# Performance work log

Hardware: AMD Instinct MI355X
Metric: run time of the kernel (lower is better)

The kernel has to match this reference:

```python
import jax, jax.numpy as jnp
import numpy as np

DIM = 2048
N_HEADS = 16
N_KV_HEADS = 4
HEAD_DIM = DIM // N_HEADS  # 128
N_REP = N_HEADS // N_KV_HEADS
MAX_SEQ_LEN = 4096
SEQLEN = 4096


def setup_inputs() -> dict:
    key = jax.random.key(0)
    ks = jax.random.split(key, 6)
    x = jax.random.normal(ks[0], (1, SEQLEN, DIM), dtype=jnp.float32)
    # rotary frequencies, llama-style theta=10000
    inv_freq = 1.0 / (10000.0 ** (np.arange(0, HEAD_DIM, 2, dtype=np.float32) / HEAD_DIM))
    t = np.arange(SEQLEN, dtype=np.float32)
    ang = np.outer(t, inv_freq)  # [S, head_dim/2]
    freqs_cos = jnp.asarray(np.cos(ang))
    freqs_sin = jnp.asarray(np.sin(ang))
    # additive causal mask [S, S]
    mask = jnp.where(jnp.tril(jnp.ones((SEQLEN, SEQLEN), dtype=bool)), 0.0, -1e9).astype(jnp.float32)
    sc = 0.02
    wq = jax.random.normal(ks[1], (DIM, N_HEADS * HEAD_DIM), dtype=jnp.float32) * sc
    wk = jax.random.normal(ks[2], (DIM, N_KV_HEADS * HEAD_DIM), dtype=jnp.float32) * sc
    wv = jax.random.normal(ks[3], (DIM, N_KV_HEADS * HEAD_DIM), dtype=jnp.float32) * sc
    wo = jax.random.normal(ks[4], (N_HEADS * HEAD_DIM, DIM), dtype=jnp.float32) * sc
    return {"x": x, "start_pos": 0, "freqs_cos": freqs_cos, "freqs_sin": freqs_sin,
            "mask": mask, "wq": wq, "wk": wk, "wv": wv, "wo": wo}


def _rope(x, cos, sin):
    # x: [b, s, h, d]; cos/sin: [s, d/2]; consecutive pairs form complex numbers
    b, s, h, d = x.shape
    xr = x.astype(jnp.float32).reshape(b, s, h, d // 2, 2)
    x1, x2 = xr[..., 0], xr[..., 1]
    c = cos[None, :, None, :]
    sn = sin[None, :, None, :]
    o1 = x1 * c - x2 * sn
    o2 = x1 * sn + x2 * c
    return jnp.stack([o1, o2], axis=-1).reshape(b, s, h, d).astype(x.dtype)


def reference(x, start_pos, freqs_cos, freqs_sin, mask, wq, wk, wv, wo):
    bsz, seqlen, _ = x.shape
    xq = (x @ wq).reshape(bsz, seqlen, N_HEADS, HEAD_DIM)
    xk = (x @ wk).reshape(bsz, seqlen, N_KV_HEADS, HEAD_DIM)
    xv = (x @ wv).reshape(bsz, seqlen, N_KV_HEADS, HEAD_DIM)
    xq = _rope(xq, freqs_cos, freqs_sin)
    xk = _rope(xk, freqs_cos, freqs_sin)
    # KV-cache append (cache is zeros before this call)
    cache_k = jnp.zeros((1, MAX_SEQ_LEN, N_KV_HEADS, HEAD_DIM), dtype=xk.dtype)
    cache_v = jnp.zeros((1, MAX_SEQ_LEN, N_KV_HEADS, HEAD_DIM), dtype=xv.dtype)
    cache_k = jax.lax.dynamic_update_slice(cache_k, xk, (0, start_pos, 0, 0))
    cache_v = jax.lax.dynamic_update_slice(cache_v, xv, (0, start_pos, 0, 0))
    keys = cache_k[:bsz, : start_pos + seqlen]    # [b, T, kvh, d]
    values = cache_v[:bsz, : start_pos + seqlen]
    # GQA repeat to full head count
    keys = jnp.repeat(keys, N_REP, axis=2)
    values = jnp.repeat(values, N_REP, axis=2)
    scale = 1.0 / jnp.sqrt(jnp.float32(HEAD_DIM))
    scores = jnp.einsum('bshd,bthd->bhst', xq, keys) * scale  # [b, h, s, T]
    scores = scores + mask[None, None, :, :]
    probs = jax.nn.softmax(scores.astype(jnp.float32), axis=-1).astype(xq.dtype)
    out = jnp.einsum('bhst,bthd->bshd', probs, values).reshape(bsz, seqlen, -1)
    return out @ wo
```

## Files before the change

### kernel.cpp

```cpp
#include <hip/hip_runtime.h>
#include <hip/hip_bf16.h>
#include <stdint.h>

#define SEQ 4096
#define DIM 2048
#define NH 16
#define NKV 4
#define HD 128
#define KVLD 1024


using frag8 = __attribute__((ext_vector_type(8))) short;
using f32x4 = __attribute__((ext_vector_type(4))) float;

union VecU { ushort u[8]; uint4 v; };

__device__ __forceinline__ float bf2f(ushort u) {
    union { uint32_t u; float f; } v; v.u = ((uint32_t)u) << 16; return v.f;
}
__device__ __forceinline__ ushort f2bf(float f) {
    union { float f; uint32_t u; } v; v.f = f;
    uint32_t r = v.u + 0x7fffu + ((v.u >> 16) & 1u);
    return (ushort)(r >> 16);
}

__device__ __forceinline__ void glds16(const void* g, void* l) {
    __builtin_amdgcn_global_load_lds(
        (const __attribute__((address_space(1))) void*)g,
        (__attribute__((address_space(3))) void*)l, 16, 0, 0);
}

__global__ __launch_bounds__(256) void cvt_kernel(
    const float* __restrict__ src, ushort* __restrict__ dst)
{
    size_t i = ((size_t)blockIdx.x * 256 + threadIdx.x) * 8;
    float4 f0 = *(const float4*)&src[i];
    float4 f1 = *(const float4*)&src[i + 4];
    VecU t;
    t.u[0] = f2bf(f0.x); t.u[1] = f2bf(f0.y); t.u[2] = f2bf(f0.z); t.u[3] = f2bf(f0.w);
    t.u[4] = f2bf(f1.x); t.u[5] = f2bf(f1.y); t.u[6] = f2bf(f1.z); t.u[7] = f2bf(f1.w);
    *(uint4*)&dst[i] = t.v;
}

__global__ __launch_bounds__(256) void convT_kernel(
    const float* __restrict__ src, ushort* __restrict__ dst, int K, int N)
{
    __shared__ ushort T[32][36];
    int r  = threadIdx.x >> 3;
    int c4 = (threadIdx.x & 7) * 4;
    int bk = blockIdx.y * 32, bn = blockIdx.x * 32;
    float4 v = *(const float4*)&src[(size_t)(bk + r) * N + bn + c4];
    T[r][c4]     = f2bf(v.x); T[r][c4 + 1] = f2bf(v.y);
    T[r][c4 + 2] = f2bf(v.z); T[r][c4 + 3] = f2bf(v.w);
    __syncthreads();
    ushort4 o;
    o.x = T[c4][r]; o.y = T[c4 + 1][r]; o.z = T[c4 + 2][r]; o.w = T[c4 + 3][r];
    *(ushort4*)&dst[(size_t)(bn + r) * K + bk + c4] = o;
}

__global__ __launch_bounds__(256) void vtrans_kernel(
    const ushort* __restrict__ src, ushort* __restrict__ dst)
{
    __shared__ ushort T[32][36];
    int r  = threadIdx.x >> 3;
    int c4 = (threadIdx.x & 7) * 4;
    int bt = blockIdx.y * 32, bd = blockIdx.x * 32;
    ushort4 v = *(const ushort4*)&src[(size_t)(bt + r) * KVLD + 512 + bd + c4];
    T[r][c4] = v.x; T[r][c4 + 1] = v.y; T[r][c4 + 2] = v.z; T[r][c4 + 3] = v.w;
    __syncthreads();
    ushort4 o;
    o.x = T[c4][r]; o.y = T[c4 + 1][r]; o.z = T[c4 + 2][r]; o.w = T[c4 + 3][r];
    *(ushort4*)&dst[(size_t)(bd + r) * SEQ + bt + c4] = o;
}

template <int CF>
__global__ __launch_bounds__(256) void gemm_tn(
    const ushort* __restrict__ A, const ushort* __restrict__ BT,
    void* __restrict__ C, int M, int N, int K)
{
    __shared__ ushort As[128 * 32];
    __shared__ ushort Bs[128 * 32];

    const int tid  = threadIdx.x;
    const int lane = tid & 63;
    const int wave = tid >> 6;
    const int bm   = blockIdx.y * 128;
    const int bn   = blockIdx.x * 128;
    const int wm   = (wave >> 1) * 64;
    const int wn   = (wave & 1) * 64;
    const int quad = lane >> 4;
    const int t16  = lane & 15;
    const int kg   = quad ^ ((t16 >> 1) & 3);

    f32x4 acc[4][4] = {};

    for (int k0 = 0; k0 < K; k0 += 32) {
        #pragma unroll
        for (int it = 0; it < 2; ++it) {
            int gid = it * 256 + tid;
            int r   = gid >> 2;
            int cs  = (gid & 3) ^ ((gid >> 3) & 3);
            glds16(&A[(size_t)(bm + r) * K + k0 + cs * 8],
                   &As[(it * 256 + wave * 64) * 8]);
            glds16(&BT[(size_t)(bn + r) * K + k0 + cs * 8],
                   &Bs[(it * 256 + wave * 64) * 8]);
        }
        __syncthreads();

        frag8 af[4], bf[4];
        #pragma unroll
        for (int i = 0; i < 4; ++i)
            af[i] = *(const frag8*)&As[(wm + i * 16 + t16) * 32 + kg * 8];
        #pragma unroll
        for (int j = 0; j < 4; ++j)
            bf[j] = *(const frag8*)&Bs[(wn + j * 16 + t16) * 32 + kg * 8];
        #pragma unroll
        for (int i = 0; i < 4; ++i)
            #pragma unroll
            for (int j = 0; j < 4; ++j)
                acc[i][j] = __builtin_amdgcn_mfma_f32_16x16x32_bf16(
                    af[i], bf[j], acc[i][j], 0, 0, 0);
        __syncthreads();
    }

    #pragma unroll
    for (int i = 0; i < 4; ++i)
        #pragma unroll
        for (int j = 0; j < 4; ++j)
            #pragma unroll
            for (int r = 0; r < 4; ++r) {
                int row = bm + wm + i * 16 + quad * 4 + r;
                int col = bn + wn + j * 16 + t16;
                if (CF) ((float*)C)[(size_t)row * N + col] = acc[i][j][r];
                else    ((ushort*)C)[(size_t)row * N + col] = f2bf(acc[i][j][r]);
            }
}

__global__ void rope_kernel(ushort* __restrict__ X, const float* __restrict__ Cos,
                            const float* __restrict__ Sin, int log2nh, int strideT,
                            float oscale)
{
    int idx = blockIdx.x * blockDim.x + threadIdx.x;
    int p = idx & 63;
    int h = (idx >> 6) & ((1 << log2nh) - 1);
    int t = idx >> (6 + log2nh);
    size_t base = (size_t)t * strideT + (size_t)h * 128 + 2 * p;
    ushort2 xv = *(ushort2*)&X[base];
    float x1 = bf2f(xv.x), x2 = bf2f(xv.y);
    float c = Cos[t * 64 + p], s = Sin[t * 64 + p];
    ushort2 ov;
    ov.x = f2bf((x1 * c - x2 * s) * oscale);
    ov.y = f2bf((x1 * s + x2 * c) * oscale);
    *(ushort2*)&X[base] = ov;
}

__global__ __launch_bounds__(256) void attn_kernel(
    const ushort* __restrict__ Q, const ushort* __restrict__ Kb,
    const ushort* __restrict__ VT, ushort* __restrict__ O)
{
    __shared__ ushort Ks[64][136];
    __shared__ ushort Vt[128][72];
    __shared__ ushort Sp[4][16][72];

    const int tid  = threadIdx.x;
    const int lane = tid & 63;
    const int wave = tid >> 6;
    const int quad = lane >> 4;
    const int t16  = lane & 15;
    const int h    = blockIdx.y;
    const int kvh  = h >> 2;

    frag8 vONE;
    #pragma unroll
    for (int i = 0; i < 8; ++i) vONE[i] = (short)0x3F80;

    #pragma unroll
    for (int qi = 0; qi < 2; ++qi) {
        const int qt = qi ? (63 - (int)blockIdx.x) : (int)blockIdx.x;
        const int q0 = qt * 64;
        const int qwave = q0 + wave * 16;
        const int qmaxw = qwave + 15;

        frag8 aQ[4];
        #pragma unroll
        for (int kk = 0; kk < 4; ++kk)
            aQ[kk] = *(const frag8*)&Q[(size_t)(qwave + t16) * DIM + h * HD + kk * 32 + quad * 8];

        f32x4 o[8] = {};
        f32x4 o9 = {0.f, 0.f, 0.f, 0.f};
        float mrow[4];
        #pragma unroll
        for (int r = 0; r < 4; ++r) mrow[r] = -30000.f;

        for (int t0 = 0; t0 <= q0 + 63; t0 += 64) {
            #pragma unroll
            for (int it = 0; it < 4; ++it) {
                int idx = tid + it * 256;
                int tt  = idx >> 4;
                int c   = (idx & 15) * 8;
                *(uint4*)&Ks[tt][c] =
                    *(const uint4*)&Kb[(size_t)(t0 + tt) * KVLD + kvh * HD + c];
            }
            #pragma unroll
            for (int it = 0; it < 4; ++it) {
                int idx = tid + it * 256;
                int d   = idx >> 3;
                int tq  = (idx & 7) * 8;
                *(uint4*)&Vt[d][tq] =
                    *(const uint4*)&VT[(size_t)(kvh * HD + d) * SEQ + t0 + tq];
            }
            __syncthreads();

            const bool hi = (t0 + 32 <= qmaxw);
            {
                f32x4 s0 = {0.f, 0.f, 0.f, 0.f};
                f32x4 s1 = {0.f, 0.f, 0.f, 0.f};
                f32x4 s2 = {0.f, 0.f, 0.f, 0.f};
                f32x4 s3 = {0.f, 0.f, 0.f, 0.f};
                #pragma unroll
                for (int kk = 0; kk < 4; ++kk) {
                    frag8 b0 = *(const frag8*)&Ks[2 * t16][kk * 32 + quad * 8];
                    frag8 b1 = *(const frag8*)&Ks[2 * t16 + 1][kk * 32 + quad * 8];
                    s0 = __builtin_amdgcn_mfma_f32_16x16x32_bf16(aQ[kk], b0, s0, 0, 0, 0);
                    s1 = __builtin_amdgcn_mfma_f32_16x16x32_bf16(aQ[kk], b1, s1, 0, 0, 0);
                }
                if (hi) {
                    #pragma unroll
                    for (int kk = 0; kk < 4; ++kk) {
                        frag8 b2 = *(const frag8*)&Ks[32 + 2 * t16][kk * 32 + quad * 8];
                        frag8 b3 = *(const frag8*)&Ks[33 + 2 * t16][kk * 32 + quad * 8];
                        s2 = __builtin_amdgcn_mfma_f32_16x16x32_bf16(aQ[kk], b2, s2, 0, 0, 0);
                        s3 = __builtin_amdgcn_mfma_f32_16x16x32_bf16(aQ[kk], b3, s3, 0, 0, 0);
                    }
                }

                const bool mLo = (t0 + 31 > qwave);
                const bool mHi = (t0 + 63 > qwave);
                float v[4][4];
                float mnew[4];
                bool trig = false;
                #pragma unroll
                for (int r = 0; r < 4; ++r) {
                    int q = qwave + quad * 4 + r;
                    float v0 = s0[r];
                    float v1 = s1[r];
                    float v2 = hi ? s2[r] : -30000.f;
                    float v3 = hi ? s3[r] : -30000.f;
                    if (mLo) {
                        if (t0 + 2 * t16 > q)      v0 = -30000.f;
                        if (t0 + 2 * t16 + 1 > q)  v1 = -30000.f;
                    }
                    if (hi && mHi) {
                        if (t0 + 32 + 2 * t16 > q) v2 = -30000.f;
                        if (t0 + 33 + 2 * t16 > q) v3 = -30000.f;
                    }
                    float rm = fmaxf(fmaxf(v0, v1), fmaxf(v2, v3));
                    rm = fmaxf(rm, __shfl_xor(rm, 1));
                    rm = fmaxf(rm, __shfl_xor(rm, 2));
                    rm = fmaxf(rm, __shfl_xor(rm, 4));
                    rm = fmaxf(rm, __shfl_xor(rm, 8));
                    mnew[r] = fmaxf(mrow[r], rm);
                    trig |= (rm > mrow[r] + 8.f);
                    v[r][0] = v0; v[r][1] = v1; v[r][2] = v2; v[r][3] = v3;
                }
                if (__any(trig)) {
                    #pragma unroll
                    for (int r = 0; r < 4; ++r) {
                        float alpha = __expf(mrow[r] - mnew[r]);
                        mrow[r] = mnew[r];
                        #pragma unroll
                        for (int j = 0; j < 8; ++j) o[j][r] *= alpha;
                        o9[r] *= alpha;
                    }
                }
                #pragma unroll
                for (int r = 0; r < 4; ++r) {
                    float e0 = __expf(v[r][0] - mrow[r]);
                    float e1 = __expf(v[r][1] - mrow[r]);
                    uint pv = (uint)f2bf(e0) | ((uint)f2bf(e1) << 16);
                    *(uint*)&Sp[wave][quad * 4 + r][2 * t16] = pv;
                    if (hi) {
                        float e2 = __expf(v[r][2] - mrow[r]);
                        float e3 = __expf(v[r][3] - mrow[r]);
                        uint ph = (uint)f2bf(e2) | ((uint)f2bf(e3) << 16);
                        *(uint*)&Sp[wave][quad * 4 + r][32 + 2 * t16] = ph;
                    }
                }

                frag8 aP0 = *(const frag8*)&Sp[wave][t16][quad * 8];
                #pragma unroll
                for (int j = 0; j < 8; ++j) {
                    frag8 bV = *(const frag8*)&Vt[j * 16 + t16][quad * 8];
                    o[j] = __builtin_amdgcn_mfma_f32_16x16x32_bf16(aP0, bV, o[j], 0, 0, 0);
                }
                o9 = __builtin_amdgcn_mfma_f32_16x16x32_bf16(aP0, vONE, o9, 0, 0, 0);
                if (hi) {
                    frag8 aP1 = *(const frag8*)&Sp[wave][t16][32 + quad * 8];
                    #pragma unroll
                    for (int j = 0; j < 8; ++j) {
                        frag8 bV = *(const frag8*)&Vt[j * 16 + t16][32 + quad * 8];
                        o[j] = __builtin_amdgcn_mfma_f32_16x16x32_bf16(aP1, bV, o[j], 0, 0, 0);
                    }
                    o9 = __builtin_amdgcn_mfma_f32_16x16x32_bf16(aP1, vONE, o9, 0, 0, 0);
                }
            }
            __syncthreads();
        }

        #pragma unroll
        for (int r = 0; r < 4; ++r) {
            float inv = 1.f / fmaxf(o9[r], 1e-20f);
            int row = qwave + quad * 4 + r;
            #pragma unroll
            for (int j = 0; j < 8; ++j)
                O[(size_t)row * DIM + h * HD + j * 16 + t16] = f2bf(o[j][r] * inv);
        }
    }
}

extern "C" void kernel_launch(void* const* d_in, const int* in_sizes, int n_in,
                              void* d_out, int out_size, void* d_ws, size_t ws_size,
                              hipStream_t stream)
{
    const float* x  = (const float*)d_in[0];
    const float* fc = (const float*)d_in[2];
    const float* fs = (const float*)d_in[3];
    const float* wq = (const float*)d_in[5];
    const float* wk = (const float*)d_in[6];
    const float* wv = (const float*)d_in[7];
    const float* wo = (const float*)d_in[8];

    ushort* Qb  = (ushort*)d_ws;
    ushort* KVb = Qb + (size_t)SEQ * DIM;
    ushort* Ab  = KVb + (size_t)SEQ * KVLD;
    ushort* WqT = Ab;
    ushort* KVT = Ab + (size_t)DIM * DIM;
    ushort* WoT = KVb;

    ushort* Xb = (ushort*)d_out;
    ushort* VT = Xb + (size_t)SEQ * DIM;

    dim3 blk(256);

    cvt_kernel<<<(SEQ * DIM) / 2048, blk, 0, stream>>>(x, Xb);
    convT_kernel<<<dim3(DIM / 32, DIM / 32), blk, 0, stream>>>(wq, WqT, DIM, DIM);
    convT_kernel<<<dim3(512 / 32, DIM / 32), blk, 0, stream>>>(wk, KVT, DIM, 512);
    convT_kernel<<<dim3(512 / 32, DIM / 32), blk, 0, stream>>>(
        wv, KVT + (size_t)512 * DIM, DIM, 512);

    gemm_tn<0><<<dim3(DIM / 128, SEQ / 128), blk, 0, stream>>>(Xb, WqT, Qb, SEQ, DIM, DIM);
    gemm_tn<0><<<dim3(KVLD / 128, SEQ / 128), blk, 0, stream>>>(Xb, KVT, KVb, SEQ, KVLD, DIM);

    rope_kernel<<<(SEQ * NH * 64) / 256, blk, 0, stream>>>(
        Qb, fc, fs, 4, DIM, 0.08838834764831845f);
    rope_kernel<<<(SEQ * NKV * 64) / 256, blk, 0, stream>>>(
        KVb, fc, fs, 2, KVLD, 1.0f);

    vtrans_kernel<<<dim3(512 / 32, SEQ / 32), blk, 0, stream>>>(KVb, VT);

    attn_kernel<<<dim3(32, NH), blk, 0, stream>>>(Qb, KVb, VT, Ab);

    convT_kernel<<<dim3(DIM / 32, DIM / 32), blk, 0, stream>>>(wo, WoT, DIM, DIM);
    gemm_tn<1><<<dim3(DIM / 128, SEQ / 128), blk, 0, stream>>>(Ab, WoT, d_out, SEQ, DIM, DIM);
}
```

Before: 502.9 us.

## Prefetch next K/V tile into registers and defer row-max reduction to rare rescale path

The attention loop now issues global loads for the next K and V tile into registers before computing the current tile, then writes them to shared memory after the current tile's MFMAs. This overlaps global memory latency with compute. The running max starts at zero and the cross-lane max reduction and rescale run only when some lane's local max exceeds the running max by a threshold, in which case exponentials are recomputed. This saves shuffles on the common path but costs extra registers and an additional barrier per tile.

```diff
diff --git a/kernel.cpp b/kernel.cpp
--- a/kernel.cpp
+++ b/kernel.cpp
@@ -174,12 +174,43 @@
     #pragma unroll
     for (int i = 0; i < 8; ++i) vONE[i] = (short)0x3F80;
 
+#define LOADREGS(T0)                                                          \
+    {                                                                         \
+        _Pragma("unroll")                                                     \
+        for (int it = 0; it < 4; ++it) {                                      \
+            int idx = tid + it * 256;                                         \
+            kreg[it] = *(const uint4*)&Kb[(size_t)((T0) + (idx >> 4)) * KVLD  \
+                                          + kvh * HD + (idx & 15) * 8];       \
+        }                                                                     \
+        _Pragma("unroll")                                                     \
+        for (int it = 0; it < 4; ++it) {                                      \
+            int idx = tid + it * 256;                                         \
+            vreg[it] = *(const uint4*)&VT[(size_t)(kvh * HD + (idx >> 3)) * SEQ \
+                                          + (T0) + (idx & 7) * 8];            \
+        }                                                                     \
+    }
+
+#define WRITELDS()                                                            \
+    {                                                                         \
+        _Pragma("unroll")                                                     \
+        for (int it = 0; it < 4; ++it) {                                      \
+            int idx = tid + it * 256;                                         \
+            *(uint4*)&Ks[idx >> 4][(idx & 15) * 8] = kreg[it];                \
+        }                                                                     \
+        _Pragma("unroll")                                                     \
+        for (int it = 0; it < 4; ++it) {                                      \
+            int idx = tid + it * 256;                                         \
+            *(uint4*)&Vt[idx >> 3][(idx & 7) * 8] = vreg[it];                 \
+        }                                                                     \
+    }
+
     #pragma unroll
     for (int qi = 0; qi < 2; ++qi) {
         const int qt = qi ? (63 - (int)blockIdx.x) : (int)blockIdx.x;
         const int q0 = qt * 64;
         const int qwave = q0 + wave * 16;
         const int qmaxw = qwave + 15;
+        const int ntiles = qt + 1;
 
         frag8 aQ[4];
         #pragma unroll
@@ -188,62 +219,80 @@
 
         f32x4 o[8] = {};
         f32x4 o9 = {0.f, 0.f, 0.f, 0.f};
-        float mrow[4];
-        #pragma unroll
-        for (int r = 0; r < 4; ++r) mrow[r] = -30000.f;
-
-        for (int t0 = 0; t0 <= q0 + 63; t0 += 64) {
-            #pragma unroll
-            for (int it = 0; it < 4; ++it) {
-                int idx = tid + it * 256;
-                int tt  = idx >> 4;
-                int c   = (idx & 15) * 8;
-                *(uint4*)&Ks[tt][c] =
-                    *(const uint4*)&Kb[(size_t)(t0 + tt) * KVLD + kvh * HD + c];
-            }
-            #pragma unroll
-            for (int it = 0; it < 4; ++it) {
-                int idx = tid + it * 256;
-                int d   = idx >> 3;
-                int tq  = (idx & 7) * 8;
-                *(uint4*)&Vt[d][tq] =
-                    *(const uint4*)&VT[(size_t)(kvh * HD + d) * SEQ + t0 + tq];
-            }
-            __syncthreads();
+        float mrow[4] = {0.f, 0.f, 0.f, 0.f};
+
+        uint4 kreg[4], vreg[4];
+
+        LOADREGS(0);
+        WRITELDS();
+        __syncthreads();
+
+        for (int ti = 0; ti < ntiles; ++ti) {
+            const int t0 = ti * 64;
+
+            if (ti + 1 < ntiles) LOADREGS((ti + 1) * 64);
 
             const bool hi = (t0 + 32 <= qmaxw);
-            {
-                f32x4 s0 = {0.f, 0.f, 0.f, 0.f};
-                f32x4 s1 = {0.f, 0.f, 0.f, 0.f};
-                f32x4 s2 = {0.f, 0.f, 0.f, 0.f};
-                f32x4 s3 = {0.f, 0.f, 0.f, 0.f};
+
+            f32x4 s0 = {0.f, 0.f, 0.f, 0.f};
+            f32x4 s1 = {0.f, 0.f, 0.f, 0.f};
+            f32x4 s2 = {0.f, 0.f, 0.f, 0.f};
+            f32x4 s3 = {0.f, 0.f, 0.f, 0.f};
+            #pragma unroll
+            for (int kk = 0; kk < 4; ++kk) {
+                frag8 b0 = *(const frag8*)&Ks[2 * t16][kk * 32 + quad * 8];
+                frag8 b1 = *(const frag8*)&Ks[2 * t16 + 1][kk * 32 + quad * 8];
+                s0 = __builtin_amdgcn_mfma_f32_16x16x32_bf16(aQ[kk], b0, s0, 0, 0, 0);
+                s1 = __builtin_amdgcn_mfma_f32_16x16x32_bf16(aQ[kk], b1, s1, 0, 0, 0);
+            }
+            if (hi) {
                 #pragma unroll
                 for (int kk = 0; kk < 4; ++kk) {
-                    frag8 b0 = *(const frag8*)&Ks[2 * t16][kk * 32 + quad * 8];
-                    frag8 b1 = *(const frag8*)&Ks[2 * t16 + 1][kk * 32 + quad * 8];
-                    s0 = __builtin_amdgcn_mfma_f32_16x16x32_bf16(aQ[kk], b0, s0, 0, 0, 0);
-                    s1 = __builtin_amdgcn_mfma_f32_16x16x32_bf16(aQ[kk], b1, s1, 0, 0, 0);
-                }
+                    frag8 b2 = *(const frag8*)&Ks[32 + 2 * t16][kk * 32 + quad * 8];
+                    frag8 b3 = *(const frag8*)&Ks[33 + 2 * t16][kk * 32 + quad * 8];
+                    s2 = __builtin_amdgcn_mfma_f32_16x16x32_bf16(aQ[kk], b2, s2, 0, 0, 0);
+                    s3 = __builtin_amdgcn_mfma_f32_16x16x32_bf16(aQ[kk], b3, s3, 0, 0, 0);
+                }
+            }
+
+            const bool mLo = (t0 + 31 > qwave);
+            const bool mHi = (t0 + 63 > qwave);
+
+            bool trig = false;
+            #pragma unroll
+            for (int r = 0; r < 4; ++r) {
+                int q = qwave + quad * 4 + r;
+                float v0 = s0[r];
+                float v1 = s1[r];
+                float v2 = hi ? s2[r] : -30000.f;
+                float v3 = hi ? s3[r] : -30000.f;
+                if (mLo) {
+                    if (t0 + 2 * t16 > q)      v0 = -30000.f;
+                    if (t0 + 2 * t16 + 1 > q)  v1 = -30000.f;
+                }
+                if (hi && mHi) {
+                    if (t0 + 32 + 2 * t16 > q) v2 = -30000.f;
+                    if (t0 + 33 + 2 * t16 > q) v3 = -30000.f;
+                }
+                float lm = fmaxf(fmaxf(v0, v1), fmaxf(v2, v3));
+                trig |= (lm > mrow[r] + 8.f);
+                float e0 = __expf(v0 - mrow[r]);
+                float e1 = __expf(v1 - mrow[r]);
+                *(uint*)&Sp[wave][quad * 4 + r][2 * t16] =
+                    (uint)f2bf(e0) | ((uint)f2bf(e1) << 16);
                 if (hi) {
-                    #pragma unroll
-                    for (int kk = 0; kk < 4; ++kk) {
-                        frag8 b2 = *(const frag8*)&Ks[32 + 2 * t16][kk * 32 + quad * 8];
-                        frag8 b3 = *(const frag8*)&Ks[33 + 2 * t16][kk * 32 + quad * 8];
-                        s2 = __builtin_amdgcn_mfma_f32_16x16x32_bf16(aQ[kk], b2, s2, 0, 0, 0);
-                        s3 = __builtin_amdgcn_mfma_f32_16x16x32_bf16(aQ[kk], b3, s3, 0, 0, 0);
-                    }
-                }
-
-                const bool mLo = (t0 + 31 > qwave);
-                const bool mHi = (t0 + 63 > qwave);
-                float v[4][4];
-                float mnew[4];
-                bool trig = false;
+                    float e2 = __expf(v2 - mrow[r]);
+                    float e3 = __expf(v3 - mrow[r]);
+                    *(uint*)&Sp[wave][quad * 4 + r][32 + 2 * t16] =
+                        (uint)f2bf(e2) | ((uint)f2bf(e3) << 16);
+                }
+            }
+
+            if (__any(trig)) {
                 #pragma unroll
                 for (int r = 0; r < 4; ++r) {
                     int q = qwave + quad * 4 + r;
-                    float v0 = s0[r];
-                    float v1 = s1[r];
+                    float v0 = s0[r], v1 = s1[r];
                     float v2 = hi ? s2[r] : -30000.f;
                     float v3 = hi ? s3[r] : -30000.f;
                     if (mLo) {
@@ -259,52 +308,47 @@
                     rm = fmaxf(rm, __shfl_xor(rm, 2));
                     rm = fmaxf(rm, __shfl_xor(rm, 4));
                     rm = fmaxf(rm, __shfl_xor(rm, 8));
-                    mnew[r] = fmaxf(mrow[r], rm);
-                    trig |= (rm > mrow[r] + 8.f);
-                    v[r][0] = v0; v[r][1] = v1; v[r][2] = v2; v[r][3] = v3;
-                }
-                if (__any(trig)) {
+                    float mnew  = fmaxf(mrow[r], rm);
+                    float alpha = __expf(mrow[r] - mnew);
                     #pragma unroll
-                    for (int r = 0; r < 4; ++r) {
-                        float alpha = __expf(mrow[r] - mnew[r]);
-                        mrow[r] = mnew[r];
-                        #pragma unroll
-                        for (int j = 0; j < 8; ++j) o[j][r] *= alpha;
-                        o9[r] *= alpha;
+                    for (int j = 0; j < 8; ++j) o[j][r] *= alpha;
+                    o9[r] *= alpha;
+                    mrow[r] = mnew;
+                    float e0 = __expf(v0 - mnew);
+                    float e1 = __expf(v1 - mnew);
+                    *(uint*)&Sp[wave][quad * 4 + r][2 * t16] =
+                        (uint)f2bf(e0) | ((uint)f2bf(e1) << 16);
+                    if (hi) {
+                        float e2 = __expf(v2 - mnew);
+                        float e3 = __expf(v3 - mnew);
+                        *(uint*)&Sp[wave][quad * 4 + r][32 + 2 * t16] =
+                            (uint)f2bf(e2) | ((uint)f2bf(e3) << 16);
                     }
                 }
-                #pragma unroll
-                for (int r = 0; r < 4; ++r) {
-                    float e0 = __expf(v[r][0] - mrow[r]);
-                    float e1 = __expf(v[r][1] - mrow[r]);
-                    uint pv = (uint)f2bf(e0) | ((uint)f2bf(e1) << 16);
-                    *(uint*)&Sp[wave][quad * 4 + r][2 * t16] = pv;
-                    if (hi) {
-                        float e2 = __expf(v[r][2] - mrow[r]);
-                        float e3 = __expf(v[r][3] - mrow[r]);
-                        uint ph = (uint)f2bf(e2) | ((uint)f2bf(e3) << 16);
-                        *(uint*)&Sp[wave][quad * 4 + r][32 + 2 * t16] = ph;
-                    }
-                }
-
-                frag8 aP0 = *(const frag8*)&Sp[wave][t16][quad * 8];
+            }
+
+            frag8 aP0 = *(const frag8*)&Sp[wave][t16][quad * 8];
+            #pragma unroll
+            for (int j = 0; j < 8; ++j) {
+                frag8 bV = *(const frag8*)&Vt[j * 16 + t16][quad * 8];
+                o[j] = __builtin_amdgcn_mfma_f32_16x16x32_bf16(aP0, bV, o[j], 0, 0, 0);
+            }
+            o9 = __builtin_amdgcn_mfma_f32_16x16x32_bf16(aP0, vONE, o9, 0, 0, 0);
+            if (hi) {
+                frag8 aP1 = *(const frag8*)&Sp[wave][t16][32 + quad * 8];
                 #pragma unroll
                 for (int j = 0; j < 8; ++j) {
-                    frag8 bV = *(const frag8*)&Vt[j * 16 + t16][quad * 8];
-                    o[j] = __builtin_amdgcn_mfma_f32_16x16x32_bf16(aP0, bV, o[j], 0, 0, 0);
-                }
-                o9 = __builtin_amdgcn_mfma_f32_16x16x32_bf16(aP0, vONE, o9, 0, 0, 0);
-                if (hi) {
-                    frag8 aP1 = *(const frag8*)&Sp[wave][t16][32 + quad * 8];
-                    #pragma unroll
-                    for (int j = 0; j < 8; ++j) {
-                        frag8 bV = *(const frag8*)&Vt[j * 16 + t16][32 + quad * 8];
-                        o[j] = __builtin_amdgcn_mfma_f32_16x16x32_bf16(aP1, bV, o[j], 0, 0, 0);
-                    }
-                    o9 = __builtin_amdgcn_mfma_f32_16x16x32_bf16(aP1, vONE, o9, 0, 0, 0);
-                }
-            }
+                    frag8 bV = *(const frag8*)&Vt[j * 16 + t16][32 + quad * 8];
+                    o[j] = __builtin_amdgcn_mfma_f32_16x16x32_bf16(aP1, bV, o[j], 0, 0, 0);
+                }
+                o9 = __builtin_amdgcn_mfma_f32_16x16x32_bf16(aP1, vONE, o9, 0, 0, 0);
+            }
+
             __syncthreads();
+            if (ti + 1 < ntiles) {
+                WRITELDS();
+                __syncthreads();
+            }
         }
 
         #pragma unroll
@@ -316,6 +360,8 @@
                 O[(size_t)row * DIM + h * HD + j * 16 + t16] = f2bf(o[j][r] * inv);
         }
     }
+#undef LOADREGS
+#undef WRITELDS
 }
 
 extern "C" void kernel_launch(void* const* d_in, const int* in_sizes, int n_in,
```

Result: slower. 664.2 us (+32.1%).
